# Optimization experiments

Hardware: AMD Instinct MI355X
Metric: run time of the kernel (lower is better)

## Reference

```python
import jax, jax.numpy as jnp
import numpy as np

N = 50000   # nodes
E = 800000  # edges (avg degree 16)
H = 3       # attention heads
D_IN, D_HID, D_OUT = 256, 64, 10


def setup_inputs() -> dict:
    key = jax.random.key(0)
    ks = jax.random.split(key, 8)
    x = jax.random.normal(ks[0], (N, D_IN), dtype=jnp.float32)
    edge_index = jax.random.randint(ks[1], (2, E), 0, N, dtype=jnp.int64)
    W1 = jax.random.normal(ks[2], (H, D_IN, D_HID), dtype=jnp.float32) / np.sqrt(D_IN)
    a_src1 = jax.random.normal(ks[3], (H, D_HID), dtype=jnp.float32) / np.sqrt(D_HID)
    a_dst1 = jax.random.normal(ks[4], (H, D_HID), dtype=jnp.float32) / np.sqrt(D_HID)
    W2 = jax.random.normal(ks[5], (H, D_HID, D_OUT), dtype=jnp.float32) / np.sqrt(D_HID)
    a_src2 = jax.random.normal(ks[6], (H, D_OUT), dtype=jnp.float32) / np.sqrt(D_OUT)
    a_dst2 = jax.random.normal(ks[7], (H, D_OUT), dtype=jnp.float32) / np.sqrt(D_OUT)
    return {"x": x, "edge_index": edge_index, "W1": W1, "a_src1": a_src1,
            "a_dst1": a_dst1, "W2": W2, "a_src2": a_src2, "a_dst2": a_dst2}


def gat_layer(x, src, dst, W, a_s, a_d, n):
    # x: [N, Din]; W: [H, Din, Dout]; returns [N, Dout] (heads averaged)
    z = jnp.einsum('nd,hde->nhe', x, W)                     # [N, H, Dout]
    e_src = jnp.einsum('nhe,he->nh', z, a_s)[src]           # [E, H]
    e_dst = jnp.einsum('nhe,he->nh', z, a_d)[dst]           # [E, H]
    e = jax.nn.leaky_relu(e_src + e_dst, 0.2)               # [E, H]
    # numerically-stable softmax over incoming edges of each dst node
    m = jax.lax.stop_gradient(jax.ops.segment_max(e, dst, num_segments=n))
    ex = jnp.exp(e - m[dst])                                # [E, H]
    denom = jax.ops.segment_sum(ex, dst, num_segments=n)    # [N, H]
    alpha = ex / (denom[dst] + 1e-16)                       # [E, H]
    out = jax.ops.segment_sum(z[src] * alpha[:, :, None], dst, num_segments=n)
    return out.mean(axis=1)                                 # [N, Dout]


def reference(x, edge_index, W1, a_src1, a_dst1, W2, a_src2, a_dst2):
    n = x.shape[0]
    src, dst = edge_index[0], edge_index[1]
    # dropout layers are identity in eval/deterministic mode
    h = gat_layer(x, src, dst, W1, a_src1, a_dst1, n)
    h = jax.nn.elu(h)
    h = gat_layer(h, src, dst, W2, a_src2, a_dst2, n)
    return h, jax.nn.log_softmax(h, axis=1)
```

## Files before the change

kernel.cpp:

```cpp
#include <hip/hip_runtime.h>
#include <math.h>

#define DIN  256
#define DHID 64
#define NH   3
#define DOUT 10
#define CAP  64

typedef __attribute__((ext_vector_type(8))) short bf16x8;
typedef __attribute__((ext_vector_type(4))) float f32x4;

__device__ inline unsigned short f2bf(float f) {
    unsigned u = __builtin_bit_cast(unsigned, f);
    unsigned r = (u + 0x7FFFu + ((u >> 16) & 1u)) >> 16;
    return (unsigned short)r;
}
__device__ inline float bf2f(unsigned short s) {
    unsigned u = ((unsigned)s) << 16;
    return __builtin_bit_cast(float, u);
}
__device__ inline f32x4 cvt4(ushort4 z) {
    f32x4 r;
    r[0] = bf2f(z.x); r[1] = bf2f(z.y); r[2] = bf2f(z.z); r[3] = bf2f(z.w);
    return r;
}

#define SCHUNK 2048


__global__ __launch_bounds__(256) void repack_scatter_kernel(
        const float* __restrict__ W1, const float* __restrict__ W2,
        unsigned short* __restrict__ W1p, float* __restrict__ W2cat,
        const int* __restrict__ src, const int* __restrict__ dst,
        int* __restrict__ cursor, unsigned short* __restrict__ esrcp,
        int E, int pbase) {
    int bid = blockIdx.x;
    int tid = threadIdx.x;
    if (bid < 192) {
        int idx = bid * 256 + tid;
        int j = idx & 7, l = (idx >> 3) & 63, q = (idx >> 9) & 7, t = idx >> 12;
        int c = t * 16 + (l & 15);
        int k = q * 32 + (l >> 4) * 8 + j;
        int h = c >> 6, jj = c & 63;
        W1p[idx] = f2bf(W1[h * 16384 + k * 64 + jj]);
    } else if (bid < 200) {
        int idx = (bid - 192) * 256 + tid;
        if (idx < 2048) {
            int kk = idx >> 5, c = idx & 31;
            float wv = 0.f;
            if (c < 30) {
                int h = c / 10, j = c % 10;
                wv = W2[(h * 64 + kk) * 10 + j];
            }
            W2cat[idx] = wv;
        }
    } else {
        int sb = bid - 200;
        int part = bid & 7;
        int base = (sb >> 3) * SCHUNK;
        int lo = part * pbase, hi = lo + pbase;
        #pragma unroll
        for (int k = 0; k < SCHUNK / 256; ++k) {
            int i = base + k * 256 + tid;
            if (i < E) {
                int d = dst[i];
                if (d >= lo && d < hi) {
                    int s = src[i];
                    int pos = atomicAdd(cursor + d, 1);
                    if (pos < CAP) esrcp[d * CAP + pos] = (unsigned short)s;
                }
            }
        }
    }
}


__global__ __launch_bounds__(128) void gemm1_mfma_kernel(const float* __restrict__ x,
                                                         const bf16x8* __restrict__ W1p,
                                                         const float* __restrict__ a_s,
                                                         const float* __restrict__ a_d,
                                                         unsigned short* __restrict__ z1bf,
                                                         float* __restrict__ s1,
                                                         float* __restrict__ d1, int n) {
    __shared__ unsigned short Xs[32][272];
    int tid = threadIdx.x;
    int w = tid >> 6, lane = tid & 63;
    int m = lane & 15, quad = lane >> 4;
    int n0 = blockIdx.x * 32;

    for (int i = tid; i < 2048; i += 128) {
        int r = i >> 6, c4 = i & 63;
        int nn = n0 + r;
        float4 a = (nn < n) ? *(const float4*)(x + (size_t)nn * 256 + c4 * 4)
                            : (float4){0.f, 0.f, 0.f, 0.f};
        ushort4 b;
        b.x = f2bf(a.x); b.y = f2bf(a.y); b.z = f2bf(a.z); b.w = f2bf(a.w);
        *(ushort4*)(&Xs[r][c4 * 4]) = b;
    }
    __syncthreads();

    int rloc = w * 16 + m;
    f32x4 acc[12];
    #pragma unroll
    for (int t = 0; t < 12; ++t) acc[t] = (f32x4){0.f, 0.f, 0.f, 0.f};
    #pragma unroll
    for (int q = 0; q < 8; ++q) {
        bf16x8 af = *(const bf16x8*)(&Xs[rloc][q * 32 + quad * 8]);
        #pragma unroll
        for (int t = 0; t < 12; ++t) {
            bf16x8 bfr = W1p[(t * 8 + q) * 64 + lane];
            acc[t] = __builtin_amdgcn_mfma_f32_16x16x32_bf16(af, bfr, acc[t], 0, 0, 0);
        }
    }
    __syncthreads();

    float as_r[12], ad_r[12];
    #pragma unroll
    for (int t = 0; t < 12; ++t) { as_r[t] = a_s[t * 16 + m]; ad_r[t] = a_d[t * 16 + m]; }

    #pragma unroll
    for (int reg = 0; reg < 4; ++reg) {
        int row_loc = w * 16 + quad * 4 + reg;
        int row_out = n0 + row_loc;
        bool ok = row_out < n;
        float ps[3] = {0.f, 0.f, 0.f}, pd[3] = {0.f, 0.f, 0.f};
        #pragma unroll
        for (int t = 0; t < 12; ++t) {
            float v = acc[t][reg];
            Xs[row_loc][t * 16 + m] = f2bf(v);
            ps[t >> 2] += v * as_r[t];
            pd[t >> 2] += v * ad_r[t];
        }
        #pragma unroll
        for (int h = 0; h < 3; ++h) {
            float s = ps[h], d = pd[h];
            #pragma unroll
            for (int msk = 1; msk < 16; msk <<= 1) {
                s += __shfl_xor(s, msk, 16);
                d += __shfl_xor(d, msk, 16);
            }
            if (ok && m == 0) { s1[row_out * 4 + h] = s; d1[row_out * 4 + h] = d; }
        }
    }
    __syncthreads();

    for (int i = tid; i < 1536; i += 128) {
        int r = i / 48, c4 = i % 48;
        int nn = n0 + r;
        if (nn < n)
            *(ushort4*)(z1bf + (size_t)nn * 192 + c4 * 4) = *(const ushort4*)(&Xs[r][c4 * 4]);
    }
}


__global__ __launch_bounds__(256) void agg1_gemm2_kernel(
        const int* __restrict__ cnts, const unsigned short* __restrict__ esrcp,
        const float* __restrict__ s1, const float* __restrict__ d1,
        const unsigned short* __restrict__ z1bf,
        const float* __restrict__ W2cat, const float* __restrict__ as2,
        const float* __restrict__ ad2,
        unsigned short* __restrict__ z2bf,
        float* __restrict__ s2, float* __restrict__ d2, int n) {
    __shared__ float Ws[64][32];
    __shared__ float wlds[4][196];
    __shared__ float hb[4][64];
    __shared__ float tb[4][64];
    int tid = threadIdx.x;
    int lane = tid & 63, wave = tid >> 6;

    for (int idx = tid; idx < 1024; idx += 256)
        ((float2*)&Ws[0][0])[idx] = ((const float2*)W2cat)[idx];
    __syncthreads();

    int v = blockIdx.x * 4 + wave;
    if (v >= n) return;
    int cnt = cnts[v]; if (cnt > CAP) cnt = CAP;
    int m16 = lane & 15;
    int grp = lane >> 4;
    int head = grp > 2 ? 2 : grp;
    bool rowact = lane < 48;
    float dv0 = d1[v * 4], dv1 = d1[v * 4 + 1], dv2 = d1[v * 4 + 2];
    float* wl = wlds[wave];

    int u_l = 0; float w0 = 0.f, w1 = 0.f, w2 = 0.f;
    if (lane < cnt) {
        u_l = (int)esrcp[v * CAP + lane];
        float4 sv = *(const float4*)(s1 + (size_t)u_l * 4);
        float e0 = sv.x + dv0; e0 = e0 > 0.f ? e0 : 0.2f * e0;
        float e1 = sv.y + dv1; e1 = e1 > 0.f ? e1 : 0.2f * e1;
        float e2 = sv.z + dv2; e2 = e2 > 0.f ? e2 : 0.2f * e2;
        w0 = __expf(e0); w1 = __expf(e1); w2 = __expf(e2);
    }
    wl[lane] = w0; wl[65 + lane] = w1; wl[130 + lane] = w2;

    f32x4 acc = (f32x4){0.f, 0.f, 0.f, 0.f};
    if (rowact) {
        int rnd = (cnt + 7) & ~7;
        const int wb = head * 65;
        ushort4 zr[8]; float wr[8];
        #pragma unroll
        for (int i = 0; i < 8; ++i) {
            int u = __builtin_amdgcn_readlane(u_l, i);
            zr[i] = *(const ushort4*)(z1bf + (size_t)u * 192 + lane * 4);
            wr[i] = wl[wb + i];
        }
        for (int j = 8; j < rnd; j += 8) {
            ushort4 zn[8]; float wn[8];
            #pragma unroll
            for (int i = 0; i < 8; ++i) {
                int u = __builtin_amdgcn_readlane(u_l, j + i);
                zn[i] = *(const ushort4*)(z1bf + (size_t)u * 192 + lane * 4);
                wn[i] = wl[wb + j + i];
            }
            #pragma unroll
            for (int i = 0; i < 8; ++i) acc += cvt4(zr[i]) * wr[i];
            #pragma unroll
            for (int i = 0; i < 8; ++i) { zr[i] = zn[i]; wr[i] = wn[i]; }
        }
        #pragma unroll
        for (int i = 0; i < 8; ++i) acc += cvt4(zr[i]) * wr[i];
    }

    float4 wv4 = *(const float4*)(&wl[head * 65 + m16 * 4]);
    float denp = wv4.x + wv4.y + wv4.z + wv4.w;
    #pragma unroll
    for (int msk = 1; msk < 16; msk <<= 1) denp += __shfl_xor(denp, msk, 16);

    float invd = (1.f / 3.f) / (denp + 1e-16f);
    float acc0 = rowact ? acc[0] * invd : 0.f;
    float acc1 = rowact ? acc[1] * invd : 0.f;
    float acc2 = rowact ? acc[2] * invd : 0.f;
    float acc3 = rowact ? acc[3] * invd : 0.f;
    acc0 += __shfl_down(acc0, 32, 64); acc0 += __shfl_down(acc0, 16, 64);
    acc1 += __shfl_down(acc1, 32, 64); acc1 += __shfl_down(acc1, 16, 64);
    acc2 += __shfl_down(acc2, 32, 64); acc2 += __shfl_down(acc2, 16, 64);
    acc3 += __shfl_down(acc3, 32, 64); acc3 += __shfl_down(acc3, 16, 64);
    if (lane < 16) {
        float4 o;
        o.x = acc0 > 0.f ? acc0 : __expf(acc0) - 1.f;
        o.y = acc1 > 0.f ? acc1 : __expf(acc1) - 1.f;
        o.z = acc2 > 0.f ? acc2 : __expf(acc2) - 1.f;
        o.w = acc3 > 0.f ? acc3 : __expf(acc3) - 1.f;
        *(float4*)(&hb[wave][lane * 4]) = o;
    }

    int c = lane & 31, half = lane >> 5;
    int k0 = half * 32;
    float zc0 = 0.f, zc1 = 0.f;
    #pragma unroll
    for (int k = 0; k < 32; k += 2) {
        zc0 += hb[wave][k0 + k]     * Ws[k0 + k][c];
        zc1 += hb[wave][k0 + k + 1] * Ws[k0 + k + 1][c];
    }
    float zc = zc0 + zc1;
    zc += __shfl_down(zc, 32, 64);
    if (lane < 32) {
        z2bf[(size_t)v * 32 + c] = f2bf(zc);
        if (c < 30) {
            tb[wave][c]      = zc * as2[c];
            tb[wave][32 + c] = zc * ad2[c];
        }
    }
    if (lane < 6) {
        int h = lane >> 1;
        int base = (lane & 1) * 32 + h * 10;
        float sum = 0.f;
        #pragma unroll
        for (int j = 0; j < 10; ++j) sum += tb[wave][base + j];
        if ((lane & 1) == 0) s2[v * 4 + h] = sum;
        else                 d2[v * 4 + h] = sum;
    }
}


__global__ __launch_bounds__(256) void agg2_kernel(const int* __restrict__ cnts,
                                                   const unsigned short* __restrict__ esrcp,
                                                   const float* __restrict__ s2,
                                                   const float* __restrict__ d2,
                                                   const unsigned short* __restrict__ z2bf,
                                                   float* __restrict__ out, int n) {
    __shared__ float wlds[4][196];
    __shared__ float dlds[4][4];
    int tid = threadIdx.x;
    int lane = tid & 63, wave = tid >> 6;
    int v = blockIdx.x * 4 + wave;
    if (v >= n) return;
    int cnt = cnts[v]; if (cnt > CAP) cnt = CAP;
    int c2 = lane & 15;
    int quad = lane >> 4;
    int headc = c2 < 5 ? 0 : (c2 < 10 ? 1 : 2);
    int headg = quad > 2 ? 2 : quad;
    float dv0 = d2[v * 4], dv1 = d2[v * 4 + 1], dv2 = d2[v * 4 + 2];
    float* wl = wlds[wave];

    int u_l = 0; float w0 = 0.f, w1 = 0.f, w2 = 0.f;
    if (lane < cnt) {
        u_l = (int)esrcp[v * CAP + lane];
        float4 sv = *(const float4*)(s2 + (size_t)u_l * 4);
        float e0 = sv.x + dv0; e0 = e0 > 0.f ? e0 : 0.2f * e0;
        float e1 = sv.y + dv1; e1 = e1 > 0.f ? e1 : 0.2f * e1;
        float e2 = sv.z + dv2; e2 = e2 > 0.f ? e2 : 0.2f * e2;
        w0 = __expf(e0); w1 = __expf(e1); w2 = __expf(e2);
    }
    wl[lane] = w0; wl[65 + lane] = w1; wl[130 + lane] = w2;

    float ax = 0.f, ay = 0.f;
    {
        int rnd = (cnt + 7) & ~7;
        const int wb = headc * 65;
        int ua = __shfl(u_l, quad, 64);
        int ub = __shfl(u_l, 4 + quad, 64);
        float wa = wl[wb + quad], wbb = wl[wb + 4 + quad];
        ushort2 za = *(const ushort2*)(z2bf + (size_t)ua * 32 + c2 * 2);
        ushort2 zb = *(const ushort2*)(z2bf + (size_t)ub * 32 + c2 * 2);
        for (int j = 8; j < rnd; j += 8) {
            int un1 = __shfl(u_l, j + quad, 64);
            int un2 = __shfl(u_l, j + 4 + quad, 64);
            float wn1 = wl[wb + j + quad], wn2 = wl[wb + j + 4 + quad];
            ushort2 zn1 = *(const ushort2*)(z2bf + (size_t)un1 * 32 + c2 * 2);
            ushort2 zn2 = *(const ushort2*)(z2bf + (size_t)un2 * 32 + c2 * 2);
            ax += wa * bf2f(za.x) + wbb * bf2f(zb.x);
            ay += wa * bf2f(za.y) + wbb * bf2f(zb.y);
            wa = wn1; wbb = wn2; za = zn1; zb = zn2;
        }
        ax += wa * bf2f(za.x) + wbb * bf2f(zb.x);
        ay += wa * bf2f(za.y) + wbb * bf2f(zb.y);
    }

    float4 wv = *(const float4*)(&wl[headg * 65 + c2 * 4]);
    float denp = wv.x + wv.y + wv.z + wv.w;
    #pragma unroll
    for (int msk = 1; msk < 16; msk <<= 1) denp += __shfl_xor(denp, msk, 16);
    if (c2 == 0 && quad < 3) dlds[wave][quad] = denp;
    float den = dlds[wave][headc];

    ax += __shfl_down(ax, 32, 64); ax += __shfl_down(ax, 16, 64);
    ay += __shfl_down(ay, 32, 64); ay += __shfl_down(ay, 16, 64);
    float inv = 1.f / (den + 1e-16f);
    float rx = ax * inv, ry = ay * inv;
    float rx5  = __shfl(rx, lane + 5, 64);
    float rx10 = __shfl(rx, lane + 10, 64);
    float ry5  = __shfl(ry, lane + 5, 64);
    float ry10 = __shfl(ry, lane + 10, 64);
    float rrx = (rx + rx5 + rx10) * (1.f / 3.f);
    float rry = (ry + ry5 + ry10) * (1.f / 3.f);
    bool act = lane < 5;
    float mx = act ? fmaxf(rrx, rry) : -1e30f;
    #pragma unroll
    for (int msk = 1; msk < 8; msk <<= 1) mx = fmaxf(mx, __shfl_xor(mx, msk, 8));
    float e = act ? (__expf(rrx - mx) + __expf(rry - mx)) : 0.f;
    #pragma unroll
    for (int msk = 1; msk < 8; msk <<= 1) e += __shfl_xor(e, msk, 8);
    float lg = __logf(e);
    if (act) {
        float2 o1; o1.x = rrx; o1.y = rry;
        float2 o2; o2.x = rrx - mx - lg; o2.y = rry - mx - lg;
        *(float2*)(out + (size_t)v * DOUT + c2 * 2) = o1;
        *(float2*)(out + (size_t)n * DOUT + (size_t)v * DOUT + c2 * 2) = o2;
    }
}


extern "C" void kernel_launch(void* const* d_in, const int* in_sizes, int n_in,
                              void* d_out, int out_size, void* d_ws, size_t ws_size,
                              hipStream_t stream) {
    const float* x   = (const float*)d_in[0];
    const int*   ei  = (const int*)d_in[1];
    const float* W1  = (const float*)d_in[2];
    const float* as1 = (const float*)d_in[3];
    const float* ad1 = (const float*)d_in[4];
    const float* W2  = (const float*)d_in[5];
    const float* as2 = (const float*)d_in[6];
    const float* ad2 = (const float*)d_in[7];
    float* out = (float*)d_out;

    const int N = in_sizes[0] / DIN;
    const int E = in_sizes[1] / 2;
    const int* src = ei;
    const int* dst = ei + E;

    char* p = (char*)d_ws;
    auto alloc = [&](size_t bytes) -> void* {
        void* r = (void*)p;
        p += (bytes + 255) & ~(size_t)255;
        return r;
    };
    int* cursor  = (int*)alloc((size_t)N * 4);
    unsigned short* esrcp = (unsigned short*)alloc((size_t)N * CAP * 2);
    unsigned short* W1p  = (unsigned short*)alloc((size_t)49152 * 2);
    float* W2cat = (float*)alloc((size_t)2048 * 4);
    unsigned short* z1bf = (unsigned short*)alloc((size_t)N * 192 * 2);
    float* s1    = (float*)alloc((size_t)N * 4 * 4);
    float* d1    = (float*)alloc((size_t)N * 4 * 4);
    unsigned short* z2bf = (unsigned short*)alloc((size_t)N * 32 * 2);
    float* s2    = (float*)alloc((size_t)N * 4 * 4);
    float* d2    = (float*)alloc((size_t)N * 4 * 4);
    (void)alloc(512);

    hipMemsetAsync(cursor, 0, (size_t)N * 4, stream);

    int pbase = (N + 7) / 8;
    int nchunks = (E + SCHUNK - 1) / SCHUNK;
    repack_scatter_kernel<<<200 + nchunks * 8, 256, 0, stream>>>(
        W1, W2, W1p, W2cat, src, dst, cursor, esrcp, E, pbase);

    gemm1_mfma_kernel<<<(N + 31) / 32, 128, 0, stream>>>(x, (const bf16x8*)W1p, as1, ad1,
                                                         z1bf, s1, d1, N);
    agg1_gemm2_kernel<<<(N + 3) / 4, 256, 0, stream>>>(cursor, esrcp, s1, d1, z1bf,
                                                       W2cat, as2, ad2, z2bf, s2, d2, N);
    agg2_kernel<<<(N + 3) / 4, 256, 0, stream>>>(cursor, esrcp, s2, d2, z2bf, out, N);
}
```

Before: 247.5 us.

## Pack layer-2 features and attention scalars into one record, prefetch gathered rows

Merges z2, s2 and d2 into a single 128-byte per-node record, so the attention scalars and features of a neighbor share cache lines. It also adds early touch loads of the neighbor rows (z1 in agg1, rec2 in agg2) while the attention weights are computed, warming the cache before the main gather. The x-to-bf16 conversion now uses the packed v_cvt_pk_bf16_f32 instruction instead of manual rounding. The risks are extra memory traffic from the prefetch loads and a doubled per-node footprint for the layer-2 features.

```diff
diff --git a/kernel.cpp b/kernel.cpp
--- a/kernel.cpp
+++ b/kernel.cpp
@@ -93,9 +93,11 @@
         int nn = n0 + r;
         float4 a = (nn < n) ? *(const float4*)(x + (size_t)nn * 256 + c4 * 4)
                             : (float4){0.f, 0.f, 0.f, 0.f};
-        ushort4 b;
-        b.x = f2bf(a.x); b.y = f2bf(a.y); b.z = f2bf(a.z); b.w = f2bf(a.w);
-        *(ushort4*)(&Xs[r][c4 * 4]) = b;
+        unsigned plo, phi;
+        asm("v_cvt_pk_bf16_f32 %0, %1, %2" : "=v"(plo) : "v"(a.x), "v"(a.y));
+        asm("v_cvt_pk_bf16_f32 %0, %1, %2" : "=v"(phi) : "v"(a.z), "v"(a.w));
+        uint2 pk; pk.x = plo; pk.y = phi;
+        *(uint2*)(&Xs[r][c4 * 4]) = pk;
     }
     __syncthreads();
 
@@ -159,8 +161,7 @@
         const unsigned short* __restrict__ z1bf,
         const float* __restrict__ W2cat, const float* __restrict__ as2,
         const float* __restrict__ ad2,
-        unsigned short* __restrict__ z2bf,
-        float* __restrict__ s2, float* __restrict__ d2, int n) {
+        unsigned short* __restrict__ rec2, int n) {
     __shared__ float Ws[64][32];
     __shared__ float wlds[4][196];
     __shared__ float hb[4][64];
@@ -183,8 +184,11 @@
     float* wl = wlds[wave];
 
     int u_l = 0; float w0 = 0.f, w1 = 0.f, w2 = 0.f;
+    unsigned pf = 0;
     if (lane < cnt) {
         u_l = (int)esrcp[v * CAP + lane];
+        const unsigned* zr = (const unsigned*)(z1bf + (size_t)u_l * 192);
+        pf = zr[0] + zr[32] + zr[64];
         float4 sv = *(const float4*)(s1 + (size_t)u_l * 4);
         float e0 = sv.x + dv0; e0 = e0 > 0.f ? e0 : 0.2f * e0;
         float e1 = sv.y + dv1; e1 = e1 > 0.f ? e1 : 0.2f * e1;
@@ -192,6 +196,7 @@
         w0 = __expf(e0); w1 = __expf(e1); w2 = __expf(e2);
     }
     wl[lane] = w0; wl[65 + lane] = w1; wl[130 + lane] = w2;
+    asm volatile("" :: "v"(pf));
 
     f32x4 acc = (f32x4){0.f, 0.f, 0.f, 0.f};
     if (rowact) {
@@ -244,6 +249,7 @@
         *(float4*)(&hb[wave][lane * 4]) = o;
     }
 
+    unsigned short* rec = rec2 + (size_t)v * 64;
     int c = lane & 31, half = lane >> 5;
     int k0 = half * 32;
     float zc0 = 0.f, zc1 = 0.f;
@@ -255,7 +261,7 @@
     float zc = zc0 + zc1;
     zc += __shfl_down(zc, 32, 64);
     if (lane < 32) {
-        z2bf[(size_t)v * 32 + c] = f2bf(zc);
+        rec[c] = f2bf(zc);
         if (c < 30) {
             tb[wave][c]      = zc * as2[c];
             tb[wave][32 + c] = zc * ad2[c];
@@ -267,17 +273,16 @@
         float sum = 0.f;
         #pragma unroll
         for (int j = 0; j < 10; ++j) sum += tb[wave][base + j];
-        if ((lane & 1) == 0) s2[v * 4 + h] = sum;
-        else                 d2[v * 4 + h] = sum;
+        float* fb = (float*)(rec + 32);
+        if ((lane & 1) == 0) fb[h] = sum;
+        else                 fb[4 + h] = sum;
     }
 }
 
 
 __global__ __launch_bounds__(256) void agg2_kernel(const int* __restrict__ cnts,
                                                    const unsigned short* __restrict__ esrcp,
-                                                   const float* __restrict__ s2,
-                                                   const float* __restrict__ d2,
-                                                   const unsigned short* __restrict__ z2bf,
+                                                   const unsigned short* __restrict__ rec2,
                                                    float* __restrict__ out, int n) {
     __shared__ float wlds[4][196];
     __shared__ float dlds[4][4];
@@ -290,19 +295,24 @@
     int quad = lane >> 4;
     int headc = c2 < 5 ? 0 : (c2 < 10 ? 1 : 2);
     int headg = quad > 2 ? 2 : quad;
-    float dv0 = d2[v * 4], dv1 = d2[v * 4 + 1], dv2 = d2[v * 4 + 2];
+    const float* myb = (const float*)(rec2 + (size_t)v * 64 + 32);
+    float dv0 = myb[4], dv1 = myb[5], dv2 = myb[6];
     float* wl = wlds[wave];
 
     int u_l = 0; float w0 = 0.f, w1 = 0.f, w2 = 0.f;
+    unsigned pf = 0;
     if (lane < cnt) {
         u_l = (int)esrcp[v * CAP + lane];
-        float4 sv = *(const float4*)(s2 + (size_t)u_l * 4);
+        const unsigned short* ru = rec2 + (size_t)u_l * 64;
+        pf = *(const unsigned*)ru;
+        float4 sv = *(const float4*)((const float*)(ru + 32));
         float e0 = sv.x + dv0; e0 = e0 > 0.f ? e0 : 0.2f * e0;
         float e1 = sv.y + dv1; e1 = e1 > 0.f ? e1 : 0.2f * e1;
         float e2 = sv.z + dv2; e2 = e2 > 0.f ? e2 : 0.2f * e2;
         w0 = __expf(e0); w1 = __expf(e1); w2 = __expf(e2);
     }
     wl[lane] = w0; wl[65 + lane] = w1; wl[130 + lane] = w2;
+    asm volatile("" :: "v"(pf));
 
     float ax = 0.f, ay = 0.f;
     {
@@ -311,14 +321,14 @@
         int ua = __shfl(u_l, quad, 64);
         int ub = __shfl(u_l, 4 + quad, 64);
         float wa = wl[wb + quad], wbb = wl[wb + 4 + quad];
-        ushort2 za = *(const ushort2*)(z2bf + (size_t)ua * 32 + c2 * 2);
-        ushort2 zb = *(const ushort2*)(z2bf + (size_t)ub * 32 + c2 * 2);
+        ushort2 za = *(const ushort2*)(rec2 + (size_t)ua * 64 + c2 * 2);
+        ushort2 zb = *(const ushort2*)(rec2 + (size_t)ub * 64 + c2 * 2);
         for (int j = 8; j < rnd; j += 8) {
             int un1 = __shfl(u_l, j + quad, 64);
             int un2 = __shfl(u_l, j + 4 + quad, 64);
             float wn1 = wl[wb + j + quad], wn2 = wl[wb + j + 4 + quad];
-            ushort2 zn1 = *(const ushort2*)(z2bf + (size_t)un1 * 32 + c2 * 2);
-            ushort2 zn2 = *(const ushort2*)(z2bf + (size_t)un2 * 32 + c2 * 2);
+            ushort2 zn1 = *(const ushort2*)(rec2 + (size_t)un1 * 64 + c2 * 2);
+            ushort2 zn2 = *(const ushort2*)(rec2 + (size_t)un2 * 64 + c2 * 2);
             ax += wa * bf2f(za.x) + wbb * bf2f(zb.x);
             ay += wa * bf2f(za.y) + wbb * bf2f(zb.y);
             wa = wn1; wbb = wn2; za = zn1; zb = zn2;
@@ -392,9 +402,7 @@
     unsigned short* z1bf = (unsigned short*)alloc((size_t)N * 192 * 2);
     float* s1    = (float*)alloc((size_t)N * 4 * 4);
     float* d1    = (float*)alloc((size_t)N * 4 * 4);
-    unsigned short* z2bf = (unsigned short*)alloc((size_t)N * 32 * 2);
-    float* s2    = (float*)alloc((size_t)N * 4 * 4);
-    float* d2    = (float*)alloc((size_t)N * 4 * 4);
+    unsigned short* rec2 = (unsigned short*)alloc((size_t)N * 64 * 2);
     (void)alloc(512);
 
     hipMemsetAsync(cursor, 0, (size_t)N * 4, stream);
@@ -407,6 +415,6 @@
     gemm1_mfma_kernel<<<(N + 31) / 32, 128, 0, stream>>>(x, (const bf16x8*)W1p, as1, ad1,
                                                          z1bf, s1, d1, N);
     agg1_gemm2_kernel<<<(N + 3) / 4, 256, 0, stream>>>(cursor, esrcp, s1, d1, z1bf,
-                                                       W2cat, as2, ad2, z2bf, s2, d2, N);
-    agg2_kernel<<<(N + 3) / 4, 256, 0, stream>>>(cursor, esrcp, s2, d2, z2bf, out, N);
-}
+                                                       W2cat, as2, ad2, rec2, N);
+    agg2_kernel<<<(N + 3) / 4, 256, 0, stream>>>(cursor, esrcp, rec2, out, N);
+}
```

Result: slower. 254.4 us (+2.8%).
